# Optimization experiments

Hardware: AMD Instinct MI355X
Metric: run time of the kernel (lower is better)

## Reference

```python
import jax, jax.numpy as jnp
import numpy as np

B, L, H, V, HALF = 128, 4096, 64, 64, 32
ALPHA = 0.95
LN_EPS = 1e-5


def _normalize(x):
    # torch F.normalize(dim=-1): x / max(||x||_2, 1e-12)
    n = jnp.linalg.norm(x, axis=-1, keepdims=True)
    return x / jnp.maximum(n, 1e-12)


def setup_inputs() -> dict:
    key = jax.random.key(0)
    ks = jax.random.split(key, 17)
    s = 0.05
    return {
        "seq": jax.random.randint(ks[0], (B, L), 0, V),
        "embed": jax.random.normal(ks[1], (V, H), jnp.float32),
        "W1": jax.random.normal(ks[2], (H, 2 * H), jnp.float32) * s,
        "b1": jnp.zeros((2 * H,), jnp.float32),
        "W2": jax.random.normal(ks[3], (2 * H, H), jnp.float32) * s,
        "b2": jnp.zeros((H,), jnp.float32),
        "gamma": jnp.ones((H,), jnp.float32),
        "beta": jnp.zeros((H,), jnp.float32),
        "Ws": jax.random.normal(ks[4], (H, HALF), jnp.float32) * s,
        "bs": jnp.zeros((HALF,), jnp.float32),
        "We": jax.random.normal(ks[5], (H, HALF), jnp.float32) * s,
        "be": jnp.zeros((HALF,), jnp.float32),
        "Wrp": jax.random.normal(ks[6], (2 * HALF, H), jnp.float32) * s,
        "brp": jnp.zeros((H,), jnp.float32),
        "Wout": jax.random.normal(ks[7], (H, V), jnp.float32) * s,
        "bout": jnp.zeros((V,), jnp.float32),
    }


def _forward(seq, embed, W1, b1, W2, b2, gamma, beta,
             Ws, bs, We, be, Wrp, brp, Wout, bout):
    # Encoder: embed + FF(ReLU) residual + LayerNorm
    h0 = embed[seq]                                   # [B,L,H]
    ff = jnp.maximum(h0 @ W1 + b1, 0.0) @ W2 + b2
    x = h0 + ff
    mu = x.mean(-1, keepdims=True)
    var = ((x - mu) ** 2).mean(-1, keepdims=True)
    h = (x - mu) / jnp.sqrt(var + LN_EPS) * gamma + beta  # [B,L,H]

    # Precompute per-step projections for t = 0 .. L-2
    hp = h[:, :-1, :]                                 # [B,L-1,H]
    hs = hp @ Ws + bs                                 # [B,L-1,HALF]
    he = hp @ We + be
    ksn = _normalize(hs)
    ken = _normalize(he)
    scale = (jnp.arange(L - 1, dtype=h.dtype) + 1.0) / L  # (t+1)/L

    def step(carry, inp):
        M_s, M_e = carry                              # [B,HALF,HALF]
        hs_t, he_t, ks_t, ke_t, sc = inp
        vps = jnp.einsum('bij,bj->bi', M_s, ks_t)
        vpe = jnp.einsum('bij,bj->bi', M_e, ke_t)
        M_s = M_s + (1.0 - ALPHA) * (hs_t - vps)[:, :, None] * ks_t[:, None, :]
        M_e = M_e + (1.0 - ALPHA) * sc * (he_t - vpe)[:, :, None] * ke_t[:, None, :]
        return (M_s, M_e), None

    xs = (jnp.swapaxes(hs, 0, 1), jnp.swapaxes(he, 0, 1),
          jnp.swapaxes(ksn, 0, 1), jnp.swapaxes(ken, 0, 1), scale)
    M0 = jnp.zeros((B, HALF, HALF), h.dtype)
    (M_s, M_e), _ = jax.lax.scan(step, (M0, M0), xs)

    # Read with last-token query
    q = h[:, -1, :]
    qs = _normalize(q @ Ws + bs)
    qe = _normalize(q @ We + be)
    rs = jnp.einsum('bij,bj->bi', M_s, qs)
    re = jnp.einsum('bij,bj->bi', M_e, qe)
    r = jnp.concatenate([rs, re], axis=-1)            # [B,2*HALF]
    return (r @ Wrp + brp) @ Wout + bout              # [B,V]


def reference(seq, embed, W1, b1, W2, b2, gamma, beta,
              Ws, bs, We, be, Wrp, brp, Wout, bout):
    return _forward(seq, embed, W1, b1, W2, b2, gamma, beta,
                    Ws, bs, We, be, Wrp, brp, Wout, bout)
```

## Files before the change

### kernel.cpp

```cpp
#include <hip/hip_runtime.h>
#include <hip/hip_bf16.h>
#include <stdint.h>


#define BETA 0.05f
#define NB 128
#define NL 4096
#define NSTEPS 4095

#define A_EMBED 0
#define A_W1    4096
#define A_B1    12288
#define A_W2    12416
#define A_B2    20608
#define A_GAMMA 20672
#define A_BETA  20736
#define A_WSM   20800
#define A_BS    22848
#define A_WEM   22880
#define A_BE    24928
#define A_WRP   24960
#define A_BRP   29056
#define A_WOUT  29120
#define A_BOUT  33216
#define A_TOTAL 33280

struct Ptrs { const void* p[15]; };

__device__ inline float readlane_f(float v, int l) {
    return __int_as_float(__builtin_amdgcn_readlane(__float_as_int(v), l));
}

__global__ __launch_bounds__(256) void convert_inputs(Ptrs ps, float* __restrict__ arena)
{
    const int sizes[15] = {4096, 8192, 128, 8192, 64, 64, 64, 2048, 32, 2048, 32, 4096, 64, 4096, 64};
    const int offs[15] = {A_EMBED, A_W1, A_B1, A_W2, A_B2, A_GAMMA, A_BETA,
                          A_WSM, A_BS, A_WEM, A_BE, A_WRP, A_BRP, A_WOUT, A_BOUT};
    uint32_t g0 = *(const uint32_t*)ps.p[5];
    int isbf = (g0 == 0x3F803F80u) ? 1 : 0;
    int t = blockIdx.x;
    const void* src = ps.p[t];
    float* dst = arena + offs[t];
    int n = sizes[t];
    if (isbf) {
        const __hip_bfloat16* s = (const __hip_bfloat16*)src;
        for (int i = threadIdx.x; i < n; i += 256) dst[i] = __bfloat162float(s[i]);
    } else {
        const float* s = (const float*)src;
        for (int i = threadIdx.x; i < n; i += 256) dst[i] = s[i];
    }
}

__global__ __launch_bounds__(64, 2) void build_tables(const float* __restrict__ A,
                                                      float* __restrict__ tbl)
{
    int v = blockIdx.x;
    int j = threadIdx.x;
    __shared__ float h0s[64];
    __shared__ float act[128];
    __shared__ float hrow[64];

    float h0 = A[A_EMBED + v * 64 + j];
    h0s[j] = h0;
    __syncthreads();

    float za = A[A_B1 + j];
    float zb = A[A_B1 + j + 64];
    for (int k = 0; k < 64; ++k) {
        float hk = h0s[k];
        za = fmaf(hk, A[A_W1 + k * 128 + j], za);
        zb = fmaf(hk, A[A_W1 + k * 128 + j + 64], zb);
    }
    act[j] = fmaxf(za, 0.0f);
    act[j + 64] = fmaxf(zb, 0.0f);
    __syncthreads();

    float ff = A[A_B2 + j];
    for (int k = 0; k < 128; ++k)
        ff = fmaf(act[k], A[A_W2 + k * 64 + j], ff);
    float x = h0 + ff;

    float s = x;
    for (int off = 32; off >= 1; off >>= 1) s += __shfl_xor(s, off, 64);
    float mu = s * (1.0f / 64.0f);
    float d = x - mu;
    float s2 = d * d;
    for (int off = 32; off >= 1; off >>= 1) s2 += __shfl_xor(s2, off, 64);
    float var = s2 * (1.0f / 64.0f);
    float h = d / sqrtf(var + 1e-5f) * A[A_GAMMA + j] + A[A_BETA + j];
    hrow[j] = h;
    __syncthreads();

    if (j < 32) {
        float sv = A[A_BS + j];
        for (int k = 0; k < 64; ++k)
            sv = fmaf(hrow[k], A[A_WSM + k * 32 + j], sv);
        float n2 = sv * sv;
        for (int off = 16; off >= 1; off >>= 1) n2 += __shfl_xor(n2, off, 64);
        float nrm = fmaxf(sqrtf(n2), 1e-12f);
        tbl[v * 32 + j] = sv;
        tbl[2048 + v * 32 + j] = sv / nrm;
    } else {
        int jj = j - 32;
        float ev = A[A_BE + jj];
        for (int k = 0; k < 64; ++k)
            ev = fmaf(hrow[k], A[A_WEM + k * 32 + jj], ev);
        float n2 = ev * ev;
        for (int off = 16; off >= 1; off >>= 1) n2 += __shfl_xor(n2, off, 64);
        float nrm = fmaxf(sqrtf(n2), 1e-12f);
        tbl[4096 + v * 32 + jj] = ev;
        tbl[6144 + v * 32 + jj] = ev / nrm;
    }
}

__global__ __launch_bounds__(64, 2) void gram_tables(const float* __restrict__ tbl,
                                                     float* __restrict__ G)
{
    int mat = blockIdx.x >> 6, vt = blockIdx.x & 63;
    int lane = threadIdx.x;
    __shared__ float K[64 * 33];
    const float* ks = tbl + 2048 + mat * 4096;
    for (int i = lane; i < 2048; i += 64)
        K[(i >> 5) * 33 + (i & 31)] = ks[i];
    __syncthreads();
    const float* kr = K + vt * 33;
    const float* kl = K + lane * 33;
    float s = 0.0f;
#pragma unroll
    for (int j = 0; j < 32; ++j) s = fmaf(kr[j], kl[j], s);
    G[(size_t)(mat * 64 + vt) * 64 + lane] = s;
}

__global__ __launch_bounds__(64, 1) void ema_scan(
    const int* __restrict__ seq, const float* __restrict__ tbl,
    const float* __restrict__ G, float* __restrict__ rvbuf)
{
    __shared__ float Gl[64 * 64];
    __shared__ float da[64];

    int bm = blockIdx.x;
    int b = bm >> 1, mat = bm & 1;
    int lane = threadIdx.x;

    const float* gs = G + (size_t)mat * 4096;
    for (int i = lane; i < 4096; i += 64) Gl[i] = gs[i];
    const int* sb = seq + (size_t)b * NL;
    int vlast = sb[NL - 1];
    int tok = sb[63 * 64 + lane];
    __syncthreads();

    float y = Gl[vlast * 64 + lane];
    float daccn = 0.0f;
    const float bstep = BETA * (1.0f / 4096.0f);

    for (int g = 63; g >= 0; --g) {
        int tokc = tok;
        if (g > 0) tok = sb[(g - 1) * 64 + lane];
        float t1 = (float)(g * 64 + lane + 1);
        float bneg = mat ? (-bstep * t1) : (-BETA);
        if (g == 63 && lane == 63) bneg = 0.0f;

        float gv[64];
#pragma unroll
        for (int s = 63; s >= 0; --s) {
            int svt = __builtin_amdgcn_readlane(tokc, s);
            float sbn = readlane_f(bneg, s);
            gv[s] = Gl[svt * 64 + lane] * sbn;
        }
#pragma unroll
        for (int s = 63; s >= 0; --s) {
            int svt = __builtin_amdgcn_readlane(tokc, s);
            float sy = readlane_f(y, svt);
            y = fmaf(sy, gv[s], y);
            float ysel = (lane == svt) ? sy : 0.0f;
            daccn = fmaf(ysel, gv[s], daccn);
        }
    }

    da[lane] = -daccn;
    __syncthreads();

    if (lane < 32) {
        const float* h = tbl + mat * 4096;
        float r = 0.0f;
        for (int v = 0; v < 64; ++v)
            r = fmaf(da[v], h[v * 32 + lane], r);
        rvbuf[(size_t)bm * 32 + lane] = r;
    }
}

__global__ __launch_bounds__(64, 2) void reduce_readout(
    const float* __restrict__ rvbuf, const float* __restrict__ A,
    const void* ln_g, void* __restrict__ outv)
{
    __shared__ float rv[64];
    __shared__ float o1s[64];
    int b = blockIdx.x;
    int tid = threadIdx.x;

    rv[tid] = rvbuf[b * 64 + tid];
    __syncthreads();
    float o = A[A_BRP + tid];
    for (int i = 0; i < 64; ++i)
        o = fmaf(rv[i], A[A_WRP + i * 64 + tid], o);
    o1s[tid] = o;
    __syncthreads();
    float o2 = A[A_BOUT + tid];
    for (int i = 0; i < 64; ++i)
        o2 = fmaf(o1s[i], A[A_WOUT + i * 64 + tid], o2);
    int isbf = (*(const uint32_t*)ln_g == 0x3F803F80u) ? 1 : 0;
    if (isbf)
        ((__hip_bfloat16*)outv)[b * 64 + tid] = __float2bfloat16(o2);
    else
        ((float*)outv)[b * 64 + tid] = o2;
}

extern "C" void kernel_launch(void* const* d_in, const int* in_sizes, int n_in,
                              void* d_out, int out_size, void* d_ws, size_t ws_size,
                              hipStream_t stream) {
    const int* seq = (const int*)d_in[0];
    Ptrs ps;
    for (int i = 0; i < 15; ++i) ps.p[i] = d_in[i + 1];
    const void* ln_g = d_in[6];

    float* arena = (float*)d_ws;
    float* tbl = arena + A_TOTAL;
    float* G = tbl + 8192;
    float* rvbuf = G + 8192;

    convert_inputs<<<15, 256, 0, stream>>>(ps, arena);
    build_tables<<<64, 64, 0, stream>>>(arena, tbl);
    gram_tables<<<128, 64, 0, stream>>>(tbl, G);
    ema_scan<<<NB * 2, 64, 0, stream>>>(seq, tbl, G, rvbuf);
    reduce_readout<<<NB, 64, 0, stream>>>(rvbuf, arena, ln_g, d_out);
}
```

Measured before the change: 224.9 us.

## Fuse conversion, Gram, scan and readout into two kernels with software-pipelined scan

Drops the input-conversion kernel by templating table building on the input dtype. The Gram matrix is now computed per block inside the scan kernel, which handles both memories with 128 threads. The readout is fused in as well, removing three launches and the global round-trips. The scan double-buffers the gathered Gram rows so the loads for the next group overlap the serial chain, and the da accumulation becomes a shared-memory atomicAdd. The cost is that every block recomputes the 64x64 Gram matrices, and the kernel carries more registers and shared memory.

```diff
diff --git a/kernel.cpp b/kernel.cpp
--- a/kernel.cpp
+++ b/kernel.cpp
@@ -6,53 +6,20 @@
 #define BETA 0.05f
 #define NB 128
 #define NL 4096
-#define NSTEPS 4095
-
-#define A_EMBED 0
-#define A_W1    4096
-#define A_B1    12288
-#define A_W2    12416
-#define A_B2    20608
-#define A_GAMMA 20672
-#define A_BETA  20736
-#define A_WSM   20800
-#define A_BS    22848
-#define A_WEM   22880
-#define A_BE    24928
-#define A_WRP   24960
-#define A_BRP   29056
-#define A_WOUT  29120
-#define A_BOUT  33216
-#define A_TOTAL 33280
 
 struct Ptrs { const void* p[15]; };
 
 __device__ inline float readlane_f(float v, int l) {
     return __int_as_float(__builtin_amdgcn_readlane(__float_as_int(v), l));
 }
-
-__global__ __launch_bounds__(256) void convert_inputs(Ptrs ps, float* __restrict__ arena)
-{
-    const int sizes[15] = {4096, 8192, 128, 8192, 64, 64, 64, 2048, 32, 2048, 32, 4096, 64, 4096, 64};
-    const int offs[15] = {A_EMBED, A_W1, A_B1, A_W2, A_B2, A_GAMMA, A_BETA,
-                          A_WSM, A_BS, A_WEM, A_BE, A_WRP, A_BRP, A_WOUT, A_BOUT};
-    uint32_t g0 = *(const uint32_t*)ps.p[5];
-    int isbf = (g0 == 0x3F803F80u) ? 1 : 0;
-    int t = blockIdx.x;
-    const void* src = ps.p[t];
-    float* dst = arena + offs[t];
-    int n = sizes[t];
-    if (isbf) {
-        const __hip_bfloat16* s = (const __hip_bfloat16*)src;
-        for (int i = threadIdx.x; i < n; i += 256) dst[i] = __bfloat162float(s[i]);
-    } else {
-        const float* s = (const float*)src;
-        for (int i = threadIdx.x; i < n; i += 256) dst[i] = s[i];
-    }
-}
-
-__global__ __launch_bounds__(64, 2) void build_tables(const float* __restrict__ A,
-                                                      float* __restrict__ tbl)
+__device__ inline float ldT(const float* p, int i) { return p[i]; }
+__device__ inline float ldT(const __hip_bfloat16* p, int i) { return __bfloat162float(p[i]); }
+
+template <typename T>
+__device__ void build_tables_body(const T* emb, const T* W1, const T* b1,
+                                  const T* W2, const T* b2, const T* gam,
+                                  const T* bet, const T* Wsm, const T* bsv,
+                                  const T* Wem, const T* bev, float* tbl)
 {
     int v = blockIdx.x;
     int j = threadIdx.x;
@@ -60,24 +27,24 @@
     __shared__ float act[128];
     __shared__ float hrow[64];
 
-    float h0 = A[A_EMBED + v * 64 + j];
+    float h0 = ldT(emb, v * 64 + j);
     h0s[j] = h0;
     __syncthreads();
 
-    float za = A[A_B1 + j];
-    float zb = A[A_B1 + j + 64];
+    float za = ldT(b1, j);
+    float zb = ldT(b1, j + 64);
     for (int k = 0; k < 64; ++k) {
         float hk = h0s[k];
-        za = fmaf(hk, A[A_W1 + k * 128 + j], za);
-        zb = fmaf(hk, A[A_W1 + k * 128 + j + 64], zb);
+        za = fmaf(hk, ldT(W1, k * 128 + j), za);
+        zb = fmaf(hk, ldT(W1, k * 128 + j + 64), zb);
     }
     act[j] = fmaxf(za, 0.0f);
     act[j + 64] = fmaxf(zb, 0.0f);
     __syncthreads();
 
-    float ff = A[A_B2 + j];
+    float ff = ldT(b2, j);
     for (int k = 0; k < 128; ++k)
-        ff = fmaf(act[k], A[A_W2 + k * 64 + j], ff);
+        ff = fmaf(act[k], ldT(W2, k * 64 + j), ff);
     float x = h0 + ff;
 
     float s = x;
@@ -87,14 +54,14 @@
     float s2 = d * d;
     for (int off = 32; off >= 1; off >>= 1) s2 += __shfl_xor(s2, off, 64);
     float var = s2 * (1.0f / 64.0f);
-    float h = d / sqrtf(var + 1e-5f) * A[A_GAMMA + j] + A[A_BETA + j];
+    float h = d / sqrtf(var + 1e-5f) * ldT(gam, j) + ldT(bet, j);
     hrow[j] = h;
     __syncthreads();
 
     if (j < 32) {
-        float sv = A[A_BS + j];
+        float sv = ldT(bsv, j);
         for (int k = 0; k < 64; ++k)
-            sv = fmaf(hrow[k], A[A_WSM + k * 32 + j], sv);
+            sv = fmaf(hrow[k], ldT(Wsm, k * 32 + j), sv);
         float n2 = sv * sv;
         for (int off = 16; off >= 1; off >>= 1) n2 += __shfl_xor(n2, off, 64);
         float nrm = fmaxf(sqrtf(n2), 1e-12f);
@@ -102,9 +69,9 @@
         tbl[2048 + v * 32 + j] = sv / nrm;
     } else {
         int jj = j - 32;
-        float ev = A[A_BE + jj];
+        float ev = ldT(bev, jj);
         for (int k = 0; k < 64; ++k)
-            ev = fmaf(hrow[k], A[A_WEM + k * 32 + jj], ev);
+            ev = fmaf(hrow[k], ldT(Wem, k * 32 + jj), ev);
         float n2 = ev * ev;
         for (int off = 16; off >= 1; off >>= 1) n2 += __shfl_xor(n2, off, 64);
         float nrm = fmaxf(sqrtf(n2), 1e-12f);
@@ -113,106 +80,195 @@
     }
 }
 
-__global__ __launch_bounds__(64, 2) void gram_tables(const float* __restrict__ tbl,
-                                                     float* __restrict__ G)
-{
-    int mat = blockIdx.x >> 6, vt = blockIdx.x & 63;
-    int lane = threadIdx.x;
-    __shared__ float K[64 * 33];
-    const float* ks = tbl + 2048 + mat * 4096;
-    for (int i = lane; i < 2048; i += 64)
-        K[(i >> 5) * 33 + (i & 31)] = ks[i];
-    __syncthreads();
-    const float* kr = K + vt * 33;
-    const float* kl = K + lane * 33;
-    float s = 0.0f;
+__global__ __launch_bounds__(64, 2) void build_tables(Ptrs ps, float* __restrict__ tbl)
+{
+    uint32_t g0 = *(const uint32_t*)ps.p[5];
+    if (g0 == 0x3F803F80u)
+        build_tables_body((const __hip_bfloat16*)ps.p[0], (const __hip_bfloat16*)ps.p[1],
+                          (const __hip_bfloat16*)ps.p[2], (const __hip_bfloat16*)ps.p[3],
+                          (const __hip_bfloat16*)ps.p[4], (const __hip_bfloat16*)ps.p[5],
+                          (const __hip_bfloat16*)ps.p[6], (const __hip_bfloat16*)ps.p[7],
+                          (const __hip_bfloat16*)ps.p[8], (const __hip_bfloat16*)ps.p[9],
+                          (const __hip_bfloat16*)ps.p[10], tbl);
+    else
+        build_tables_body((const float*)ps.p[0], (const float*)ps.p[1],
+                          (const float*)ps.p[2], (const float*)ps.p[3],
+                          (const float*)ps.p[4], (const float*)ps.p[5],
+                          (const float*)ps.p[6], (const float*)ps.p[7],
+                          (const float*)ps.p[8], (const float*)ps.p[9],
+                          (const float*)ps.p[10], tbl);
+}
+
+__device__ inline float mk_tfv(int g, int lane, int mat)
+{
+    int t1 = g * 64 + lane + 1;
+    float f = mat ? (float)t1 : 1.0f;
+    if (t1 == NL) f = 0.0f;
+    return f;
+}
+
+#define LOADGV(dst, tokv, tfv)                                         \
+    { _Pragma("unroll")                                                \
+      for (int s_ = 0; s_ < 64; ++s_) {                                \
+          int rv_ = __builtin_amdgcn_readlane((tokv), s_);             \
+          float g_ = GlM[rv_ * 64 + lane];                             \
+          float t_ = readlane_f((tfv), s_);                            \
+          (dst)[s_] = g_ * t_;                                         \
+      } }
+
+#define CHAIN(gv, tokv)                                                \
+    { _Pragma("unroll")                                                \
+      for (int s_ = 63; s_ >= 0; --s_) {                               \
+          int svt_ = __builtin_amdgcn_readlane((tokv), s_);            \
+          float sy_ = readlane_f(y, svt_);                             \
+          y = fmaf(sy_, (gv)[s_], y);                                  \
+          csave = (lane == s_) ? sy_ : csave;                          \
+      } }
+
+#define DAUPD(tokv, tfv)                                               \
+    { float dv_ = csave * (bfac * (tfv));                              \
+      atomicAdd(&daL[mat * 64 + (tokv)], dv_); }
+
+__global__ __launch_bounds__(128, 1) void ema_scan_fused(
+    const int* __restrict__ seq, const float* __restrict__ tbl,
+    Ptrs ps, void* __restrict__ outv)
+{
+    __shared__ float Gl[2 * 4096];
+    __shared__ float K[2 * 64 * 36];
+    __shared__ float daL[128];
+    __shared__ float rv[64];
+    __shared__ float o1s[64];
+
+    int b = blockIdx.x;
+    int tid = threadIdx.x;
+    int mat = tid >> 6;
+    int lane = tid & 63;
+
+    daL[tid] = 0.0f;
+
+    const float4* ksrc = (const float4*)(tbl + 2048 + mat * 4096);
+    float* Km = K + mat * 64 * 36;
+    for (int i = lane; i < 512; i += 64) {
+        float4 kv = ksrc[i];
+        int vv = i >> 3, j = (i & 7) * 4;
+        float* kd = Km + vv * 36 + j;
+        kd[0] = kv.x; kd[1] = kv.y; kd[2] = kv.z; kd[3] = kv.w;
+    }
+
+    float Kown[32];
+    {
+        const float4* kr = (const float4*)(Km + lane * 36);
 #pragma unroll
-    for (int j = 0; j < 32; ++j) s = fmaf(kr[j], kl[j], s);
-    G[(size_t)(mat * 64 + vt) * 64 + lane] = s;
-}
-
-__global__ __launch_bounds__(64, 1) void ema_scan(
-    const int* __restrict__ seq, const float* __restrict__ tbl,
-    const float* __restrict__ G, float* __restrict__ rvbuf)
-{
-    __shared__ float Gl[64 * 64];
-    __shared__ float da[64];
-
-    int bm = blockIdx.x;
-    int b = bm >> 1, mat = bm & 1;
-    int lane = threadIdx.x;
-
-    const float* gs = G + (size_t)mat * 4096;
-    for (int i = lane; i < 4096; i += 64) Gl[i] = gs[i];
+        for (int j = 0; j < 8; ++j) {
+            float4 t = kr[j];
+            Kown[4 * j + 0] = t.x; Kown[4 * j + 1] = t.y;
+            Kown[4 * j + 2] = t.z; Kown[4 * j + 3] = t.w;
+        }
+    }
+
     const int* sb = seq + (size_t)b * NL;
     int vlast = sb[NL - 1];
-    int tok = sb[63 * 64 + lane];
-    __syncthreads();
-
-    float y = Gl[vlast * 64 + lane];
-    float daccn = 0.0f;
-    const float bstep = BETA * (1.0f / 4096.0f);
-
-    for (int g = 63; g >= 0; --g) {
-        int tokc = tok;
-        if (g > 0) tok = sb[(g - 1) * 64 + lane];
-        float t1 = (float)(g * 64 + lane + 1);
-        float bneg = mat ? (-bstep * t1) : (-BETA);
-        if (g == 63 && lane == 63) bneg = 0.0f;
-
-        float gv[64];
+    float bfac = mat ? (BETA / 4096.0f) : BETA;
+    float* GlM = Gl + mat * 4096;
+
+    float y = 0.0f;
+#pragma unroll 2
+    for (int vt = 0; vt < 64; ++vt) {
+        const float4* rr = (const float4*)(Km + vt * 36);
+        float acc = 0.0f;
 #pragma unroll
-        for (int s = 63; s >= 0; --s) {
-            int svt = __builtin_amdgcn_readlane(tokc, s);
-            float sbn = readlane_f(bneg, s);
-            gv[s] = Gl[svt * 64 + lane] * sbn;
-        }
-#pragma unroll
-        for (int s = 63; s >= 0; --s) {
-            int svt = __builtin_amdgcn_readlane(tokc, s);
-            float sy = readlane_f(y, svt);
-            y = fmaf(sy, gv[s], y);
-            float ysel = (lane == svt) ? sy : 0.0f;
-            daccn = fmaf(ysel, gv[s], daccn);
-        }
-    }
-
-    da[lane] = -daccn;
-    __syncthreads();
-
-    if (lane < 32) {
-        const float* h = tbl + mat * 4096;
+        for (int j = 0; j < 8; ++j) {
+            float4 t = rr[j];
+            acc = fmaf(t.x, Kown[4 * j + 0], acc);
+            acc = fmaf(t.y, Kown[4 * j + 1], acc);
+            acc = fmaf(t.z, Kown[4 * j + 2], acc);
+            acc = fmaf(t.w, Kown[4 * j + 3], acc);
+        }
+        GlM[vt * 64 + lane] = acc * (-bfac);
+        if (vt == vlast) y = acc;
+    }
+
+    float csave = 0.0f;
+    float gvA[64], gvB[64];
+    int tcur = sb[63 * 64 + lane];
+    float tfvA = mk_tfv(63, lane, mat);
+    LOADGV(gvA, tcur, tfvA)
+    int tnext = sb[62 * 64 + lane];
+    float tfvB = mk_tfv(62, lane, mat);
+    asm volatile("" ::: "memory");
+
+#pragma unroll 1
+    for (int i = 0; i < 32; ++i) {
+        int gB = 62 - 2 * i;
+        int gN = gB - 1;
+        LOADGV(gvB, tnext, tfvB)
+        asm volatile("" ::: "memory");
+        CHAIN(gvA, tcur)
+        DAUPD(tcur, tfvA)
+        int tnn = 0; float tfvN = 0.0f;
+        if (gN >= 0) {
+            tnn = sb[gN * 64 + lane];
+            tfvN = mk_tfv(gN, lane, mat);
+            LOADGV(gvA, tnn, tfvN)
+        }
+        asm volatile("" ::: "memory");
+        CHAIN(gvB, tnext)
+        DAUPD(tnext, tfvB)
+        tcur = tnn; tfvA = tfvN;
+        if (gN >= 1) {
+            tnext = sb[(gN - 1) * 64 + lane];
+            tfvB = mk_tfv(gN - 1, lane, mat);
+        }
+    }
+
+    __syncthreads();
+
+    if (tid < 64) {
+        int half = tid >> 5;
+        int j = tid & 31;
+        const float* hsrc = tbl + half * 4096;
+        const float* dv = daL + half * 64;
         float r = 0.0f;
         for (int v = 0; v < 64; ++v)
-            r = fmaf(da[v], h[v * 32 + lane], r);
-        rvbuf[(size_t)bm * 32 + lane] = r;
-    }
-}
-
-__global__ __launch_bounds__(64, 2) void reduce_readout(
-    const float* __restrict__ rvbuf, const float* __restrict__ A,
-    const void* ln_g, void* __restrict__ outv)
-{
-    __shared__ float rv[64];
-    __shared__ float o1s[64];
-    int b = blockIdx.x;
-    int tid = threadIdx.x;
-
-    rv[tid] = rvbuf[b * 64 + tid];
-    __syncthreads();
-    float o = A[A_BRP + tid];
-    for (int i = 0; i < 64; ++i)
-        o = fmaf(rv[i], A[A_WRP + i * 64 + tid], o);
-    o1s[tid] = o;
-    __syncthreads();
-    float o2 = A[A_BOUT + tid];
-    for (int i = 0; i < 64; ++i)
-        o2 = fmaf(o1s[i], A[A_WOUT + i * 64 + tid], o2);
-    int isbf = (*(const uint32_t*)ln_g == 0x3F803F80u) ? 1 : 0;
-    if (isbf)
-        ((__hip_bfloat16*)outv)[b * 64 + tid] = __float2bfloat16(o2);
-    else
-        ((float*)outv)[b * 64 + tid] = o2;
+            r = fmaf(dv[v], hsrc[v * 32 + j], r);
+        rv[tid] = r;
+    }
+    __syncthreads();
+
+    uint32_t g0 = *(const uint32_t*)ps.p[5];
+    int isbf = (g0 == 0x3F803F80u) ? 1 : 0;
+    if (tid < 64) {
+        float o;
+        if (isbf) {
+            const __hip_bfloat16* W = (const __hip_bfloat16*)ps.p[11];
+            o = __bfloat162float(((const __hip_bfloat16*)ps.p[12])[tid]);
+            for (int i = 0; i < 64; ++i)
+                o = fmaf(rv[i], __bfloat162float(W[i * 64 + tid]), o);
+        } else {
+            const float* W = (const float*)ps.p[11];
+            o = ((const float*)ps.p[12])[tid];
+            for (int i = 0; i < 64; ++i)
+                o = fmaf(rv[i], W[i * 64 + tid], o);
+        }
+        o1s[tid] = o;
+    }
+    __syncthreads();
+    if (tid < 64) {
+        float o2;
+        if (isbf) {
+            const __hip_bfloat16* W = (const __hip_bfloat16*)ps.p[13];
+            o2 = __bfloat162float(((const __hip_bfloat16*)ps.p[14])[tid]);
+            for (int i = 0; i < 64; ++i)
+                o2 = fmaf(o1s[i], __bfloat162float(W[i * 64 + tid]), o2);
+            ((__hip_bfloat16*)outv)[b * 64 + tid] = __float2bfloat16(o2);
+        } else {
+            const float* W = (const float*)ps.p[13];
+            o2 = ((const float*)ps.p[14])[tid];
+            for (int i = 0; i < 64; ++i)
+                o2 = fmaf(o1s[i], W[i * 64 + tid], o2);
+            ((float*)outv)[b * 64 + tid] = o2;
+        }
+    }
 }
 
 extern "C" void kernel_launch(void* const* d_in, const int* in_sizes, int n_in,
@@ -221,16 +277,9 @@
     const int* seq = (const int*)d_in[0];
     Ptrs ps;
     for (int i = 0; i < 15; ++i) ps.p[i] = d_in[i + 1];
-    const void* ln_g = d_in[6];
-
-    float* arena = (float*)d_ws;
-    float* tbl = arena + A_TOTAL;
-    float* G = tbl + 8192;
-    float* rvbuf = G + 8192;
-
-    convert_inputs<<<15, 256, 0, stream>>>(ps, arena);
-    build_tables<<<64, 64, 0, stream>>>(arena, tbl);
-    gram_tables<<<128, 64, 0, stream>>>(tbl, G);
-    ema_scan<<<NB * 2, 64, 0, stream>>>(seq, tbl, G, rvbuf);
-    reduce_readout<<<NB, 64, 0, stream>>>(rvbuf, arena, ln_g, d_out);
-}
+
+    float* tbl = (float*)d_ws;
+
+    build_tables<<<64, 64, 0, stream>>>(ps, tbl);
+    ema_scan_fused<<<NB, 128, 0, stream>>>(seq, tbl, ps, d_out);
+}
```

Result: slower. 277.2 us (+23.3%).
